# Kernel tuning notes

Hardware: AMD Instinct MI355X
Metric: run time of the kernel (lower is better)

The kernel has to match this reference:

```python
import jax, jax.numpy as jnp
import numpy as np

N = 50000
E = 600000
IN_DIM = 256
H1, H2, H3 = 128, 64, 64
HEADS = 8


def _add_self_loops(edge_index, edge_weight=None):
    loop = jnp.arange(N, dtype=edge_index.dtype)
    src = jnp.concatenate([edge_index[0], loop])
    dst = jnp.concatenate([edge_index[1], loop])
    if edge_weight is None:
        return src, dst, None
    ew = jnp.concatenate([edge_weight, jnp.ones((N,), edge_weight.dtype)])
    return src, dst, ew


def gcn_conv(x, edge_index, edge_weight, W, b):
    # PyG GCNConv: add self-loops (weight 1), symmetric normalization, scatter-add.
    src, dst, ew = _add_self_loops(edge_index, edge_weight)
    deg = jax.ops.segment_sum(ew, dst, num_segments=N)          # [N]
    dinv = jnp.where(deg > 0, jax.lax.rsqrt(jnp.maximum(deg, 1e-12)), 0.0)
    coeff = dinv[src] * ew * dinv[dst]                          # [E+N]
    h = x @ W                                                    # [N, out]
    out = jax.ops.segment_sum(coeff[:, None] * h[src], dst, num_segments=N)
    return out + b


def gat_conv(x, edge_index, W, att_src, att_dst, b):
    # PyG GATConv, heads=HEADS, concat=False (mean over heads), leaky_relu slope 0.2.
    src, dst, _ = _add_self_loops(edge_index)
    C = W.shape[1] // HEADS
    h = (x @ W).reshape(N, HEADS, C)                             # [N,H,C]
    a_s = jnp.sum(h * att_src, axis=-1)                          # [N,H]
    a_d = jnp.sum(h * att_dst, axis=-1)                          # [N,H]
    e = jax.nn.leaky_relu(a_s[src] + a_d[dst], negative_slope=0.2)  # [E',H]
    # scatter-softmax over edges sharing a destination
    m = jax.ops.segment_max(e, dst, num_segments=N)              # [N,H]
    p = jnp.exp(e - m[dst])
    s = jax.ops.segment_sum(p, dst, num_segments=N)              # [N,H]
    alpha = p / (s[dst] + 1e-16)                                 # [E',H]
    out = jax.ops.segment_sum(alpha[:, :, None] * h[src], dst, num_segments=N)  # [N,H,C]
    return jnp.mean(out, axis=1) + b


def setup_inputs() -> dict:
    key = jax.random.key(0)
    ks = jax.random.split(key, 12)
    x = jax.random.normal(ks[0], (N, IN_DIM), dtype=jnp.float32)
    edge_index = jax.random.randint(ks[1], (2, E), 0, N, dtype=jnp.int32)
    edge_weight = jax.random.uniform(ks[2], (E,), dtype=jnp.float32)
    def glorot(k, shape):
        fan = shape[0] + shape[-1]
        return jax.random.normal(k, shape, dtype=jnp.float32) * np.sqrt(2.0 / fan)
    return {
        "x": x, "edge_index": edge_index, "edge_weight": edge_weight,
        "gc1_w": glorot(ks[3], (IN_DIM, H1)), "gc1_b": jnp.zeros((H1,), jnp.float32),
        "gat_w": glorot(ks[4], (H1, HEADS * H2)),
        "att_src": glorot(ks[5], (HEADS, H2)), "att_dst": glorot(ks[6], (HEADS, H2)),
        "gat_b": jnp.zeros((H2,), jnp.float32),
        "gc2_w": glorot(ks[7], (H2, H3)), "gc2_b": jnp.zeros((H3,), jnp.float32),
        "fc_w": glorot(ks[8], (H3, 1)), "fc_b": jnp.zeros((1,), jnp.float32),
    }


def reference(x, edge_index, edge_weight, gc1_w, gc1_b, gat_w, att_src, att_dst,
              gat_b, gc2_w, gc2_b, fc_w, fc_b):
    # dropout is inference no-op
    h = jax.nn.relu(gcn_conv(x, edge_index, edge_weight, gc1_w, gc1_b))
    h = jax.nn.relu(gat_conv(h, edge_index, gat_w, att_src, att_dst, gat_b))
    h = jax.nn.relu(gcn_conv(h, edge_index, edge_weight, gc2_w, gc2_b))
    return h @ fc_w + fc_b                                       # [N,1]
```

## Files before the change

### kernel.cpp

```cpp
#include <hip/hip_runtime.h>
#include <hip/hip_bf16.h>

#define GNN_N 50000
#define GNN_E 600000

typedef unsigned int uint;
typedef unsigned short ushort;
using short8 = __attribute__((ext_vector_type(8))) short;
using f32x4  = __attribute__((ext_vector_type(4))) float;

__device__ __forceinline__ float leaky02(float x) { return x > 0.f ? x : 0.2f * x; }
__device__ __forceinline__ ushort f2b(float f) {
    uint u = __float_as_uint(f);
    return (ushort)((u + 0x7fffu + ((u >> 16) & 1u)) >> 16);
}
__device__ __forceinline__ float b2f(ushort b) { return __uint_as_float(((uint)b) << 16); }

__global__ void gnn_deg_init(float* deg, int n) {
    int i = blockIdx.x * blockDim.x + threadIdx.x;
    if (i < n) deg[i] = 1.0f;
}
__global__ void gnn_hist(const int* __restrict__ dst, const float* __restrict__ ew,
                         int* __restrict__ cnt, float* __restrict__ deg, int e) {
    int i = blockIdx.x * blockDim.x + threadIdx.x;
    if (i >= e) return;
    int d = dst[i];
    atomicAdd(&cnt[d], 1);
    atomicAdd(&deg[d], ew[i]);
}
__global__ void gnn_deg_fin(float* deg, int n) {
    int i = blockIdx.x * blockDim.x + threadIdx.x;
    if (i < n) deg[i] = rsqrtf(deg[i]);
}
__global__ void gnn_scan1(const int* __restrict__ cnt, int* __restrict__ row_ptr,
                          int* __restrict__ blksum, int n) {
    __shared__ int sh[256];
    int tid = threadIdx.x;
    int base = blockIdx.x * 1024 + tid * 4;
    int v0 = (base + 0 < n) ? cnt[base + 0] : 0;
    int v1 = (base + 1 < n) ? cnt[base + 1] : 0;
    int v2 = (base + 2 < n) ? cnt[base + 2] : 0;
    int v3 = (base + 3 < n) ? cnt[base + 3] : 0;
    int tsum = v0 + v1 + v2 + v3;
    sh[tid] = tsum;
    __syncthreads();
    for (int off = 1; off < 256; off <<= 1) {
        int t = (tid >= off) ? sh[tid - off] : 0;
        __syncthreads();
        sh[tid] += t;
        __syncthreads();
    }
    int excl = sh[tid] - tsum;
    if (base + 0 < n) row_ptr[base + 0] = excl; excl += v0;
    if (base + 1 < n) row_ptr[base + 1] = excl; excl += v1;
    if (base + 2 < n) row_ptr[base + 2] = excl; excl += v2;
    if (base + 3 < n) row_ptr[base + 3] = excl;
    if (tid == 255) blksum[blockIdx.x] = sh[255];
}
__global__ void gnn_scan2(int* blksum, int nblk, int* row_ptr_end, int total) {
    if (threadIdx.x == 0 && blockIdx.x == 0) {
        int run = 0;
        for (int b = 0; b < nblk; ++b) { int t = blksum[b]; blksum[b] = run; run += t; }
        *row_ptr_end = total;
    }
}
__global__ void gnn_scan3(int* row_ptr, const int* __restrict__ blksum, int n) {
    int i = blockIdx.x * blockDim.x + threadIdx.x;
    if (i < n) row_ptr[i] += blksum[i >> 10];
}
__global__ void gnn_scatter(const int* __restrict__ src, const int* __restrict__ dst,
                            const float* __restrict__ ew, const float* __restrict__ dinv,
                            const int* __restrict__ row_ptr, int* __restrict__ fill,
                            int* __restrict__ esrc, float* __restrict__ ecw, int e) {
    int i = blockIdx.x * blockDim.x + threadIdx.x;
    if (i >= e) return;
    int d = dst[i];
    int s = src[i];
    int pos = row_ptr[d] + atomicAdd(&fill[d], 1);
    esrc[pos] = s;
    ecw[pos] = dinv[s] * ew[i] * dinv[d];
}

__global__ void gnn_cast_bf16(const float* __restrict__ in, ushort* __restrict__ out, int n4) {
    int i = blockIdx.x * 256 + threadIdx.x;
    if (i >= n4) return;
    float4 v = ((const float4*)in)[i];
    ushort4 o;
    o.x = f2b(v.x); o.y = f2b(v.y); o.z = f2b(v.z); o.w = f2b(v.w);
    ((ushort4*)out)[i] = o;
}
__global__ void gnn_transpose_cast(const float* __restrict__ B, ushort* __restrict__ Bt,
                                   int K, int N) {
    int idx = blockIdx.x * 256 + threadIdx.x;
    if (idx >= K * N) return;
    int k = idx / N, n = idx - k * N;
    Bt[(size_t)n * K + k] = f2b(B[idx]);
}
__global__ void gnn_fold_att(const float* __restrict__ W, const float* __restrict__ att_src,
                             const float* __restrict__ att_dst, float* __restrict__ wa_t) {
    int t = blockIdx.x * 256 + threadIdx.x;
    if (t >= 16 * 128) return;
    int j = t >> 7;
    int k = t & 127;
    int h = j & 7;
    const float* av = (j < 8) ? att_src : att_dst;
    float s = 0.f;
    for (int c = 0; c < 64; ++c) s += W[(size_t)k * 512 + h * 64 + c] * av[h * 64 + c];
    wa_t[j * 128 + k] = s;
}

__global__ __launch_bounds__(256) void gnn_mfma_gemm(const ushort* __restrict__ A,
                                                     const ushort* __restrict__ Bt,
                                                     ushort* __restrict__ C,
                                                     int M, int N, int K) {
    __shared__ ushort As[64 * 40];
    __shared__ ushort Bs[64 * 40];
    const int tid = threadIdx.x;
    const int wv = tid >> 6, lane = tid & 63;
    const int g = lane >> 4, r = lane & 15;
    const int brow = blockIdx.y << 6, bcol = blockIdx.x << 6;

    const int srow = tid >> 2;
    const int skoff = (tid & 3) << 3;
    int arow = brow + srow;
    if (arow >= M) arow = M - 1;
    const ushort* Ap = A + (size_t)arow * K + skoff;
    const ushort* Bp = Bt + (size_t)(bcol + srow) * K + skoff;
    ushort* AsW = &As[srow * 40 + skoff];
    ushort* BsW = &Bs[srow * 40 + skoff];

    f32x4 acc[4] = {};

    for (int k0 = 0; k0 < K; k0 += 32) {
        *(short8*)AsW = *(const short8*)(Ap + k0);
        *(short8*)BsW = *(const short8*)(Bp + k0);
        __syncthreads();
        short8 bfrag = *(const short8*)&Bs[(wv * 16 + r) * 40 + g * 8];
#pragma unroll
        for (int mb = 0; mb < 4; ++mb) {
            short8 afrag = *(const short8*)&As[(mb * 16 + r) * 40 + g * 8];
            acc[mb] = __builtin_amdgcn_mfma_f32_16x16x32_bf16(afrag, bfrag, acc[mb], 0, 0, 0);
        }
        __syncthreads();
    }

    const int col = bcol + wv * 16 + r;
#pragma unroll
    for (int mb = 0; mb < 4; ++mb) {
        int rowb = brow + mb * 16 + g * 4;
#pragma unroll
        for (int rr = 0; rr < 4; ++rr) {
            int row = rowb + rr;
            if (row < M) C[(size_t)row * N + col] = f2b(acc[mb][rr]);
        }
    }
}

__global__ __launch_bounds__(256) void gnn_gcn_node128_asd(const int* __restrict__ row_ptr,
                                                           const int* __restrict__ esrc,
                                                           const float* __restrict__ ecw,
                                                           const float* __restrict__ dinv,
                                                           const ushort* __restrict__ hb,
                                                           const float* __restrict__ b,
                                                           const float* __restrict__ wa,
                                                           ushort* __restrict__ out,
                                                           float* __restrict__ a_s,
                                                           float* __restrict__ a_d, int n) {
    __shared__ float swa[16 * 128];
    for (int i = threadIdx.x; i < 16 * 128; i += 256) swa[i] = wa[i];
    __syncthreads();
    int v = blockIdx.x * 4 + (threadIdx.x >> 6);
    int lane = threadIdx.x & 63;
    if (v >= n) return;
    float di = dinv[v];
    float sc = di * di;
    uint us = *(const uint*)(hb + (size_t)v * 128 + 2 * lane);
    float acc0 = sc * __uint_as_float(us << 16);
    float acc1 = sc * __uint_as_float(us & 0xffff0000u);
    int beg = row_ptr[v], end = row_ptr[v + 1];
    int p = beg;
    for (; p + 4 <= end; p += 4) {
        int s0 = esrc[p], s1 = esrc[p + 1], s2 = esrc[p + 2], s3 = esrc[p + 3];
        float c0 = ecw[p], c1 = ecw[p + 1], c2 = ecw[p + 2], c3 = ecw[p + 3];
        uint u0 = *(const uint*)(hb + (size_t)s0 * 128 + 2 * lane);
        uint u1 = *(const uint*)(hb + (size_t)s1 * 128 + 2 * lane);
        uint u2 = *(const uint*)(hb + (size_t)s2 * 128 + 2 * lane);
        uint u3 = *(const uint*)(hb + (size_t)s3 * 128 + 2 * lane);
        acc0 += c0 * __uint_as_float(u0 << 16) + c1 * __uint_as_float(u1 << 16) +
                c2 * __uint_as_float(u2 << 16) + c3 * __uint_as_float(u3 << 16);
        acc1 += c0 * __uint_as_float(u0 & 0xffff0000u) + c1 * __uint_as_float(u1 & 0xffff0000u) +
                c2 * __uint_as_float(u2 & 0xffff0000u) + c3 * __uint_as_float(u3 & 0xffff0000u);
    }
    for (; p < end; ++p) {
        int s = esrc[p];
        float cw = ecw[p];
        uint u = *(const uint*)(hb + (size_t)s * 128 + 2 * lane);
        acc0 += cw * __uint_as_float(u << 16);
        acc1 += cw * __uint_as_float(u & 0xffff0000u);
    }
    float o0 = acc0 + b[2 * lane];
    float o1 = acc1 + b[2 * lane + 1];
    o0 = o0 > 0.f ? o0 : 0.f;
    o1 = o1 > 0.f ? o1 : 0.f;
    uint o = (uint)f2b(o0) | ((uint)f2b(o1) << 16);
    *(uint*)(out + (size_t)v * 128 + 2 * lane) = o;

    float part[16];
#pragma unroll
    for (int j = 0; j < 16; ++j)
        part[j] = o0 * swa[j * 128 + 2 * lane] + o1 * swa[j * 128 + 2 * lane + 1];
#pragma unroll
    for (int m = 1; m < 64; m <<= 1) {
#pragma unroll
        for (int j = 0; j < 16; ++j) part[j] += __shfl_xor(part[j], m);
    }
    if (lane == 0) {
#pragma unroll
        for (int j = 0; j < 8; ++j) {
            a_s[(size_t)v * 8 + j] = part[j];
            a_d[(size_t)v * 8 + j] = part[8 + j];
        }
    }
}

__global__ __launch_bounds__(256) void gnn_gat_node2(const int* __restrict__ row_ptr,
                                                     const int* __restrict__ esrc,
                                                     const float* __restrict__ a_s,
                                                     const float* __restrict__ a_d,
                                                     const ushort* __restrict__ h2,
                                                     const float* __restrict__ gat_b,
                                                     ushort* __restrict__ out, int n) {
    int v = blockIdx.x * 4 + (threadIdx.x >> 6);
    int lane = threadIdx.x & 63;
    if (v >= n) return;
    const int hd = lane >> 3;
    const float adh = a_d[(size_t)v * 8 + hd];

    float vh[8];
    float sl;
    {
        float ps = __expf(leaky02(a_s[(size_t)v * 8 + hd] + adh));
        short8 q = *(const short8*)(h2 + (size_t)v * 512 + lane * 8);
        sl = ps;
#pragma unroll
        for (int j = 0; j < 8; ++j) vh[j] = ps * b2f((ushort)q[j]);
    }
    int beg = row_ptr[v], end = row_ptr[v + 1];
    int p = beg;
    for (; p + 4 <= end; p += 4) {
        int s0 = esrc[p], s1 = esrc[p + 1], s2 = esrc[p + 2], s3 = esrc[p + 3];
        float e0 = a_s[(size_t)s0 * 8 + hd];
        float e1 = a_s[(size_t)s1 * 8 + hd];
        float e2 = a_s[(size_t)s2 * 8 + hd];
        float e3 = a_s[(size_t)s3 * 8 + hd];
        short8 q0 = *(const short8*)(h2 + (size_t)s0 * 512 + lane * 8);
        short8 q1 = *(const short8*)(h2 + (size_t)s1 * 512 + lane * 8);
        short8 q2 = *(const short8*)(h2 + (size_t)s2 * 512 + lane * 8);
        short8 q3 = *(const short8*)(h2 + (size_t)s3 * 512 + lane * 8);
        float p0 = __expf(leaky02(e0 + adh));
        float p1 = __expf(leaky02(e1 + adh));
        float p2 = __expf(leaky02(e2 + adh));
        float p3 = __expf(leaky02(e3 + adh));
        sl += (p0 + p1) + (p2 + p3);
#pragma unroll
        for (int j = 0; j < 8; ++j)
            vh[j] += p0 * b2f((ushort)q0[j]) + p1 * b2f((ushort)q1[j]) +
                     p2 * b2f((ushort)q2[j]) + p3 * b2f((ushort)q3[j]);
    }
    for (; p < end; ++p) {
        int s = esrc[p];
        float pp = __expf(leaky02(a_s[(size_t)s * 8 + hd] + adh));
        short8 q = *(const short8*)(h2 + (size_t)s * 512 + lane * 8);
        sl += pp;
#pragma unroll
        for (int j = 0; j < 8; ++j) vh[j] += pp * b2f((ushort)q[j]);
    }
    float rs = 1.f / (sl + 1e-16f);
#pragma unroll
    for (int j = 0; j < 8; ++j) vh[j] *= rs;
#pragma unroll
    for (int m = 8; m < 64; m <<= 1) {
#pragma unroll
        for (int j = 0; j < 8; ++j) vh[j] += __shfl_xor(vh[j], m);
    }
    if (lane < 8) {
        short8 o;
#pragma unroll
        for (int j = 0; j < 8; ++j) {
            float t = 0.125f * vh[j] + gat_b[lane * 8 + j];
            t = t > 0.f ? t : 0.f;
            o[j] = (short)f2b(t);
        }
        *(short8*)(out + (size_t)v * 64 + lane * 8) = o;
    }
}

__global__ __launch_bounds__(256) void gnn_gcn_node64_fc(const int* __restrict__ row_ptr,
                                                         const int* __restrict__ esrc,
                                                         const float* __restrict__ ecw,
                                                         const float* __restrict__ dinv,
                                                         const ushort* __restrict__ hb,
                                                         const float* __restrict__ b,
                                                         const float* __restrict__ fc_w,
                                                         const float* __restrict__ fc_b,
                                                         float* __restrict__ out, int n) {
    int v = blockIdx.x * 4 + (threadIdx.x >> 6);
    int lane = threadIdx.x & 63;
    if (v >= n) return;
    float di = dinv[v];
    float acc = di * di * b2f(hb[(size_t)v * 64 + lane]);
    int beg = row_ptr[v], end = row_ptr[v + 1];
    int p = beg;
    for (; p + 4 <= end; p += 4) {
        int s0 = esrc[p], s1 = esrc[p + 1], s2 = esrc[p + 2], s3 = esrc[p + 3];
        float c0 = ecw[p], c1 = ecw[p + 1], c2 = ecw[p + 2], c3 = ecw[p + 3];
        float h0 = b2f(hb[(size_t)s0 * 64 + lane]);
        float h1 = b2f(hb[(size_t)s1 * 64 + lane]);
        float h2v = b2f(hb[(size_t)s2 * 64 + lane]);
        float h3v = b2f(hb[(size_t)s3 * 64 + lane]);
        acc += c0 * h0 + c1 * h1 + c2 * h2v + c3 * h3v;
    }
    for (; p < end; ++p) {
        int s = esrc[p];
        acc += ecw[p] * b2f(hb[(size_t)s * 64 + lane]);
    }
    float o = acc + b[lane];
    o = o > 0.f ? o : 0.f;
    float val = o * fc_w[lane];
#pragma unroll
    for (int m = 32; m; m >>= 1) val += __shfl_xor(val, m);
    if (lane == 0) out[v] = val + fc_b[0];
}

extern "C" void kernel_launch(void* const* d_in, const int* in_sizes, int n_in,
                              void* d_out, int out_size, void* d_ws, size_t ws_size,
                              hipStream_t stream) {
    const float* x       = (const float*)d_in[0];
    const int*   ei      = (const int*)d_in[1];
    const float* ew      = (const float*)d_in[2];
    const float* gc1_w   = (const float*)d_in[3];
    const float* gc1_b   = (const float*)d_in[4];
    const float* gat_w   = (const float*)d_in[5];
    const float* att_src = (const float*)d_in[6];
    const float* att_dst = (const float*)d_in[7];
    const float* gat_b   = (const float*)d_in[8];
    const float* gc2_w   = (const float*)d_in[9];
    const float* gc2_b   = (const float*)d_in[10];
    const float* fc_w    = (const float*)d_in[11];
    const float* fc_b    = (const float*)d_in[12];
    float* out = (float*)d_out;

    const int N = GNN_N;
    const int E = in_sizes[2];
    const int* src = ei;
    const int* dst = ei + E;

    char* p = (char*)d_ws;
    ushort* h2b = (ushort*)p; p += (size_t)N * 512 * 2;
    ushort* xb  = (ushort*)p; p += (size_t)N * 256 * 2;
    ushort* h1b = (ushort*)p; p += (size_t)N * 128 * 2;
    ushort* g1b = (ushort*)p; p += (size_t)N * 128 * 2;
    ushort* g2b = (ushort*)p; p += (size_t)N * 64 * 2;
    ushort* h3b = (ushort*)p; p += (size_t)N * 64 * 2;
    ushort* w1t = (ushort*)p; p += (size_t)128 * 256 * 2;
    ushort* w2t = (ushort*)p; p += (size_t)512 * 128 * 2;
    ushort* w3t = (ushort*)p; p += (size_t)64 * 64 * 2;
    float*  wa_t = (float*)p; p += 16 * 128 * 4;
    float*  a_s = (float*)p;  p += (size_t)N * 8 * 4;
    float*  a_d = (float*)p;  p += (size_t)N * 8 * 4;
    float*  dinv = (float*)p; p += (size_t)N * 4;
    int* row_ptr = (int*)p;   p += (size_t)(N + 64) * 4;
    int* esrc = (int*)p;      p += (size_t)E * 4;
    float* ecw = (float*)p;   p += (size_t)E * 4;
    int* cnt = (int*)p;       p += (size_t)N * 4;
    int* fill = (int*)p;      p += (size_t)N * 4;
    int* blksum = (int*)p;    p += 4096;

    auto cdiv = [](long a, long b) { return (int)((a + b - 1) / b); };

    hipMemsetAsync(cnt, 0, (size_t)N * 8, stream);
    gnn_deg_init<<<cdiv(N, 256), 256, 0, stream>>>(dinv, N);
    gnn_hist<<<cdiv(E, 256), 256, 0, stream>>>(dst, ew, cnt, dinv, E);
    gnn_deg_fin<<<cdiv(N, 256), 256, 0, stream>>>(dinv, N);
    const int nblk = cdiv(N, 1024);
    gnn_scan1<<<nblk, 256, 0, stream>>>(cnt, row_ptr, blksum, N);
    gnn_scan2<<<1, 64, 0, stream>>>(blksum, nblk, row_ptr + N, E);
    gnn_scan3<<<cdiv(N, 256), 256, 0, stream>>>(row_ptr, blksum, N);
    gnn_scatter<<<cdiv(E, 256), 256, 0, stream>>>(src, dst, ew, dinv, row_ptr, fill, esrc, ecw, E);

    gnn_cast_bf16<<<cdiv((long)N * 256 / 4, 256), 256, 0, stream>>>(x, xb, N * 256 / 4);
    gnn_transpose_cast<<<cdiv(256 * 128, 256), 256, 0, stream>>>(gc1_w, w1t, 256, 128);
    gnn_transpose_cast<<<cdiv(128 * 512, 256), 256, 0, stream>>>(gat_w, w2t, 128, 512);
    gnn_transpose_cast<<<cdiv(64 * 64, 256), 256, 0, stream>>>(gc2_w, w3t, 64, 64);
    gnn_fold_att<<<8, 256, 0, stream>>>(gat_w, att_src, att_dst, wa_t);

    {
        dim3 grid(128 / 64, cdiv(N, 64));
        gnn_mfma_gemm<<<grid, 256, 0, stream>>>(xb, w1t, h1b, N, 128, 256);
    }
    gnn_gcn_node128_asd<<<cdiv(N, 4), 256, 0, stream>>>(row_ptr, esrc, ecw, dinv, h1b, gc1_b,
                                                        wa_t, g1b, a_s, a_d, N);

    {
        dim3 grid(512 / 64, cdiv(N, 64));
        gnn_mfma_gemm<<<grid, 256, 0, stream>>>(g1b, w2t, h2b, N, 512, 128);
    }
    gnn_gat_node2<<<cdiv(N, 4), 256, 0, stream>>>(row_ptr, esrc, a_s, a_d, h2b, gat_b, g2b, N);

    {
        dim3 grid(1, cdiv(N, 64));
        gnn_mfma_gemm<<<grid, 256, 0, stream>>>(g2b, w3t, h3b, N, 64, 64);
    }
    gnn_gcn_node64_fc<<<cdiv(N, 4), 256, 0, stream>>>(row_ptr, esrc, ecw, dinv, h3b, gc2_b,
                                                      fc_w, fc_b, out, N);
}
```

Before: 385.7 us.

## Fuse fp32-to-bf16 cast into first GEMM, merge prep kernels, unroll gathers by eight

The first GEMM now loads fp32 x directly and converts it to bf16 while staging into shared memory, which removes the separate cast kernel and its bf16 copy of x. The three weight transposes and the attention fold are merged into one prep kernel. The degree-init kernel is replaced by a wider memset, with the self-loop weight added in deg_fin. The gather loops in the three aggregation kernels are unrolled to eight edges to keep more loads in flight, at the cost of more registers per thread.

```diff
diff --git a/kernel.cpp b/kernel.cpp
--- a/kernel.cpp
+++ b/kernel.cpp
@@ -16,10 +16,6 @@
 }
 __device__ __forceinline__ float b2f(ushort b) { return __uint_as_float(((uint)b) << 16); }
 
-__global__ void gnn_deg_init(float* deg, int n) {
-    int i = blockIdx.x * blockDim.x + threadIdx.x;
-    if (i < n) deg[i] = 1.0f;
-}
 __global__ void gnn_hist(const int* __restrict__ dst, const float* __restrict__ ew,
                          int* __restrict__ cnt, float* __restrict__ deg, int e) {
     int i = blockIdx.x * blockDim.x + threadIdx.x;
@@ -30,7 +26,7 @@
 }
 __global__ void gnn_deg_fin(float* deg, int n) {
     int i = blockIdx.x * blockDim.x + threadIdx.x;
-    if (i < n) deg[i] = rsqrtf(deg[i]);
+    if (i < n) deg[i] = rsqrtf(1.0f + deg[i]);
 }
 __global__ void gnn_scan1(const int* __restrict__ cnt, int* __restrict__ row_ptr,
                           int* __restrict__ blksum, int n) {
@@ -81,35 +77,42 @@
     ecw[pos] = dinv[s] * ew[i] * dinv[d];
 }
 
-__global__ void gnn_cast_bf16(const float* __restrict__ in, ushort* __restrict__ out, int n4) {
-    int i = blockIdx.x * 256 + threadIdx.x;
-    if (i >= n4) return;
-    float4 v = ((const float4*)in)[i];
-    ushort4 o;
-    o.x = f2b(v.x); o.y = f2b(v.y); o.z = f2b(v.z); o.w = f2b(v.w);
-    ((ushort4*)out)[i] = o;
-}
-__global__ void gnn_transpose_cast(const float* __restrict__ B, ushort* __restrict__ Bt,
-                                   int K, int N) {
-    int idx = blockIdx.x * 256 + threadIdx.x;
-    if (idx >= K * N) return;
-    int k = idx / N, n = idx - k * N;
-    Bt[(size_t)n * K + k] = f2b(B[idx]);
-}
-__global__ void gnn_fold_att(const float* __restrict__ W, const float* __restrict__ att_src,
-                             const float* __restrict__ att_dst, float* __restrict__ wa_t) {
+__global__ void gnn_prep(const float* __restrict__ gc1_w, const float* __restrict__ gat_w,
+                         const float* __restrict__ gc2_w, const float* __restrict__ att_src,
+                         const float* __restrict__ att_dst, ushort* __restrict__ w1t,
+                         ushort* __restrict__ w2t, ushort* __restrict__ w3t,
+                         float* __restrict__ wa_t) {
     int t = blockIdx.x * 256 + threadIdx.x;
-    if (t >= 16 * 128) return;
-    int j = t >> 7;
-    int k = t & 127;
-    int h = j & 7;
-    const float* av = (j < 8) ? att_src : att_dst;
-    float s = 0.f;
-    for (int c = 0; c < 64; ++c) s += W[(size_t)k * 512 + h * 64 + c] * av[h * 64 + c];
-    wa_t[j * 128 + k] = s;
-}
-
-__global__ __launch_bounds__(256) void gnn_mfma_gemm(const ushort* __restrict__ A,
+    if (t < 32768) {
+        int k = t >> 7, n = t & 127;
+        w1t[n * 256 + k] = f2b(gc1_w[t]);
+        return;
+    }
+    t -= 32768;
+    if (t < 65536) {
+        int k = t >> 9, n = t & 511;
+        w2t[n * 128 + k] = f2b(gat_w[t]);
+        return;
+    }
+    t -= 65536;
+    if (t < 4096) {
+        int k = t >> 6, n = t & 63;
+        w3t[n * 64 + k] = f2b(gc2_w[t]);
+        return;
+    }
+    t -= 4096;
+    if (t < 2048) {
+        int j = t >> 7, k = t & 127;
+        int h = j & 7;
+        const float* av = (j < 8) ? att_src : att_dst;
+        float s = 0.f;
+        for (int c = 0; c < 64; ++c) s += gat_w[(size_t)k * 512 + h * 64 + c] * av[h * 64 + c];
+        wa_t[j * 128 + k] = s;
+    }
+}
+
+template <bool AF32>
+__global__ __launch_bounds__(256) void gnn_mfma_gemm(const void* __restrict__ Av,
                                                      const ushort* __restrict__ Bt,
                                                      ushort* __restrict__ C,
                                                      int M, int N, int K) {
@@ -124,7 +127,10 @@
     const int skoff = (tid & 3) << 3;
     int arow = brow + srow;
     if (arow >= M) arow = M - 1;
-    const ushort* Ap = A + (size_t)arow * K + skoff;
+    const ushort* A16 = (const ushort*)Av;
+    const float*  A32 = (const float*)Av;
+    const ushort* Ap16 = A16 + (size_t)arow * K + skoff;
+    const float*  Ap32 = A32 + (size_t)arow * K + skoff;
     const ushort* Bp = Bt + (size_t)(bcol + srow) * K + skoff;
     ushort* AsW = &As[srow * 40 + skoff];
     ushort* BsW = &Bs[srow * 40 + skoff];
@@ -132,7 +138,18 @@
     f32x4 acc[4] = {};
 
     for (int k0 = 0; k0 < K; k0 += 32) {
-        *(short8*)AsW = *(const short8*)(Ap + k0);
+        if constexpr (AF32) {
+            float4 f0 = *(const float4*)(Ap32 + k0);
+            float4 f1 = *(const float4*)(Ap32 + k0 + 4);
+            short8 t;
+            t[0] = (short)f2b(f0.x); t[1] = (short)f2b(f0.y);
+            t[2] = (short)f2b(f0.z); t[3] = (short)f2b(f0.w);
+            t[4] = (short)f2b(f1.x); t[5] = (short)f2b(f1.y);
+            t[6] = (short)f2b(f1.z); t[7] = (short)f2b(f1.w);
+            *(short8*)AsW = t;
+        } else {
+            *(short8*)AsW = *(const short8*)(Ap16 + k0);
+        }
         *(short8*)BsW = *(const short8*)(Bp + k0);
         __syncthreads();
         short8 bfrag = *(const short8*)&Bs[(wv * 16 + r) * 40 + g * 8];
@@ -179,17 +196,19 @@
     float acc1 = sc * __uint_as_float(us & 0xffff0000u);
     int beg = row_ptr[v], end = row_ptr[v + 1];
     int p = beg;
-    for (; p + 4 <= end; p += 4) {
-        int s0 = esrc[p], s1 = esrc[p + 1], s2 = esrc[p + 2], s3 = esrc[p + 3];
-        float c0 = ecw[p], c1 = ecw[p + 1], c2 = ecw[p + 2], c3 = ecw[p + 3];
-        uint u0 = *(const uint*)(hb + (size_t)s0 * 128 + 2 * lane);
-        uint u1 = *(const uint*)(hb + (size_t)s1 * 128 + 2 * lane);
-        uint u2 = *(const uint*)(hb + (size_t)s2 * 128 + 2 * lane);
-        uint u3 = *(const uint*)(hb + (size_t)s3 * 128 + 2 * lane);
-        acc0 += c0 * __uint_as_float(u0 << 16) + c1 * __uint_as_float(u1 << 16) +
-                c2 * __uint_as_float(u2 << 16) + c3 * __uint_as_float(u3 << 16);
-        acc1 += c0 * __uint_as_float(u0 & 0xffff0000u) + c1 * __uint_as_float(u1 & 0xffff0000u) +
-                c2 * __uint_as_float(u2 & 0xffff0000u) + c3 * __uint_as_float(u3 & 0xffff0000u);
+    for (; p + 8 <= end; p += 8) {
+        int s[8]; float c[8]; uint u[8];
+#pragma unroll
+        for (int t = 0; t < 8; ++t) s[t] = esrc[p + t];
+#pragma unroll
+        for (int t = 0; t < 8; ++t) c[t] = ecw[p + t];
+#pragma unroll
+        for (int t = 0; t < 8; ++t) u[t] = *(const uint*)(hb + (size_t)s[t] * 128 + 2 * lane);
+#pragma unroll
+        for (int t = 0; t < 8; ++t) {
+            acc0 += c[t] * __uint_as_float(u[t] << 16);
+            acc1 += c[t] * __uint_as_float(u[t] & 0xffff0000u);
+        }
     }
     for (; p < end; ++p) {
         int s = esrc[p];
@@ -247,25 +266,38 @@
     }
     int beg = row_ptr[v], end = row_ptr[v + 1];
     int p = beg;
-    for (; p + 4 <= end; p += 4) {
-        int s0 = esrc[p], s1 = esrc[p + 1], s2 = esrc[p + 2], s3 = esrc[p + 3];
-        float e0 = a_s[(size_t)s0 * 8 + hd];
-        float e1 = a_s[(size_t)s1 * 8 + hd];
-        float e2 = a_s[(size_t)s2 * 8 + hd];
-        float e3 = a_s[(size_t)s3 * 8 + hd];
-        short8 q0 = *(const short8*)(h2 + (size_t)s0 * 512 + lane * 8);
-        short8 q1 = *(const short8*)(h2 + (size_t)s1 * 512 + lane * 8);
-        short8 q2 = *(const short8*)(h2 + (size_t)s2 * 512 + lane * 8);
-        short8 q3 = *(const short8*)(h2 + (size_t)s3 * 512 + lane * 8);
-        float p0 = __expf(leaky02(e0 + adh));
-        float p1 = __expf(leaky02(e1 + adh));
-        float p2 = __expf(leaky02(e2 + adh));
-        float p3 = __expf(leaky02(e3 + adh));
-        sl += (p0 + p1) + (p2 + p3);
-#pragma unroll
-        for (int j = 0; j < 8; ++j)
-            vh[j] += p0 * b2f((ushort)q0[j]) + p1 * b2f((ushort)q1[j]) +
-                     p2 * b2f((ushort)q2[j]) + p3 * b2f((ushort)q3[j]);
+    for (; p + 8 <= end; p += 8) {
+        int s[8]; float e[8]; short8 q[8];
+#pragma unroll
+        for (int t = 0; t < 8; ++t) s[t] = esrc[p + t];
+#pragma unroll
+        for (int t = 0; t < 8; ++t) e[t] = a_s[(size_t)s[t] * 8 + hd];
+#pragma unroll
+        for (int t = 0; t < 8; ++t) q[t] = *(const short8*)(h2 + (size_t)s[t] * 512 + lane * 8);
+#pragma unroll
+        for (int t = 0; t < 8; ++t) {
+            float pp = __expf(leaky02(e[t] + adh));
+            sl += pp;
+#pragma unroll
+            for (int j = 0; j < 8; ++j) vh[j] += pp * b2f((ushort)q[t][j]);
+        }
+    }
+    if (p + 4 <= end) {
+        int s[4]; float e[4]; short8 q[4];
+#pragma unroll
+        for (int t = 0; t < 4; ++t) s[t] = esrc[p + t];
+#pragma unroll
+        for (int t = 0; t < 4; ++t) e[t] = a_s[(size_t)s[t] * 8 + hd];
+#pragma unroll
+        for (int t = 0; t < 4; ++t) q[t] = *(const short8*)(h2 + (size_t)s[t] * 512 + lane * 8);
+#pragma unroll
+        for (int t = 0; t < 4; ++t) {
+            float pp = __expf(leaky02(e[t] + adh));
+            sl += pp;
+#pragma unroll
+            for (int j = 0; j < 8; ++j) vh[j] += pp * b2f((ushort)q[t][j]);
+        }
+        p += 4;
     }
     for (; p < end; ++p) {
         int s = esrc[p];
@@ -311,14 +343,16 @@
     float acc = di * di * b2f(hb[(size_t)v * 64 + lane]);
     int beg = row_ptr[v], end = row_ptr[v + 1];
     int p = beg;
-    for (; p + 4 <= end; p += 4) {
-        int s0 = esrc[p], s1 = esrc[p + 1], s2 = esrc[p + 2], s3 = esrc[p + 3];
-        float c0 = ecw[p], c1 = ecw[p + 1], c2 = ecw[p + 2], c3 = ecw[p + 3];
-        float h0 = b2f(hb[(size_t)s0 * 64 + lane]);
-        float h1 = b2f(hb[(size_t)s1 * 64 + lane]);
-        float h2v = b2f(hb[(size_t)s2 * 64 + lane]);
-        float h3v = b2f(hb[(size_t)s3 * 64 + lane]);
-        acc += c0 * h0 + c1 * h1 + c2 * h2v + c3 * h3v;
+    for (; p + 8 <= end; p += 8) {
+        int s[8]; float c[8]; ushort hv[8];
+#pragma unroll
+        for (int t = 0; t < 8; ++t) s[t] = esrc[p + t];
+#pragma unroll
+        for (int t = 0; t < 8; ++t) c[t] = ecw[p + t];
+#pragma unroll
+        for (int t = 0; t < 8; ++t) hv[t] = hb[(size_t)s[t] * 64 + lane];
+#pragma unroll
+        for (int t = 0; t < 8; ++t) acc += c[t] * b2f(hv[t]);
     }
     for (; p < end; ++p) {
         int s = esrc[p];
@@ -357,7 +391,6 @@
 
     char* p = (char*)d_ws;
     ushort* h2b = (ushort*)p; p += (size_t)N * 512 * 2;
-    ushort* xb  = (ushort*)p; p += (size_t)N * 256 * 2;
     ushort* h1b = (ushort*)p; p += (size_t)N * 128 * 2;
     ushort* g1b = (ushort*)p; p += (size_t)N * 128 * 2;
     ushort* g2b = (ushort*)p; p += (size_t)N * 64 * 2;
@@ -368,18 +401,17 @@
     float*  wa_t = (float*)p; p += 16 * 128 * 4;
     float*  a_s = (float*)p;  p += (size_t)N * 8 * 4;
     float*  a_d = (float*)p;  p += (size_t)N * 8 * 4;
-    float*  dinv = (float*)p; p += (size_t)N * 4;
     int* row_ptr = (int*)p;   p += (size_t)(N + 64) * 4;
     int* esrc = (int*)p;      p += (size_t)E * 4;
     float* ecw = (float*)p;   p += (size_t)E * 4;
     int* cnt = (int*)p;       p += (size_t)N * 4;
     int* fill = (int*)p;      p += (size_t)N * 4;
+    float* dinv = (float*)p;  p += (size_t)N * 4;
     int* blksum = (int*)p;    p += 4096;
 
     auto cdiv = [](long a, long b) { return (int)((a + b - 1) / b); };
 
-    hipMemsetAsync(cnt, 0, (size_t)N * 8, stream);
-    gnn_deg_init<<<cdiv(N, 256), 256, 0, stream>>>(dinv, N);
+    hipMemsetAsync(cnt, 0, (size_t)N * 12, stream);
     gnn_hist<<<cdiv(E, 256), 256, 0, stream>>>(dst, ew, cnt, dinv, E);
     gnn_deg_fin<<<cdiv(N, 256), 256, 0, stream>>>(dinv, N);
     const int nblk = cdiv(N, 1024);
@@ -388,28 +420,24 @@
     gnn_scan3<<<cdiv(N, 256), 256, 0, stream>>>(row_ptr, blksum, N);
     gnn_scatter<<<cdiv(E, 256), 256, 0, stream>>>(src, dst, ew, dinv, row_ptr, fill, esrc, ecw, E);
 
-    gnn_cast_bf16<<<cdiv((long)N * 256 / 4, 256), 256, 0, stream>>>(x, xb, N * 256 / 4);
-    gnn_transpose_cast<<<cdiv(256 * 128, 256), 256, 0, stream>>>(gc1_w, w1t, 256, 128);
-    gnn_transpose_cast<<<cdiv(128 * 512, 256), 256, 0, stream>>>(gat_w, w2t, 128, 512);
-    gnn_transpose_cast<<<cdiv(64 * 64, 256), 256, 0, stream>>>(gc2_w, w3t, 64, 64);
-    gnn_fold_att<<<8, 256, 0, stream>>>(gat_w, att_src, att_dst, wa_t);
+    gnn_prep<<<408, 256, 0, stream>>>(gc1_w, gat_w, gc2_w, att_src, att_dst, w1t, w2t, w3t, wa_t);
 
     {
         dim3 grid(128 / 64, cdiv(N, 64));
-        gnn_mfma_gemm<<<grid, 256, 0, stream>>>(xb, w1t, h1b, N, 128, 256);
+        gnn_mfma_gemm<true><<<grid, 256, 0, stream>>>(x, w1t, h1b, N, 128, 256);
     }
     gnn_gcn_node128_asd<<<cdiv(N, 4), 256, 0, stream>>>(row_ptr, esrc, ecw, dinv, h1b, gc1_b,
                                                         wa_t, g1b, a_s, a_d, N);
 
     {
         dim3 grid(512 / 64, cdiv(N, 64));
-        gnn_mfma_gemm<<<grid, 256, 0, stream>>>(g1b, w2t, h2b, N, 512, 128);
+        gnn_mfma_gemm<false><<<grid, 256, 0, stream>>>(g1b, w2t, h2b, N, 512, 128);
     }
     gnn_gat_node2<<<cdiv(N, 4), 256, 0, stream>>>(row_ptr, esrc, a_s, a_d, h2b, gat_b, g2b, N);
 
     {
         dim3 grid(1, cdiv(N, 64));
-        gnn_mfma_gemm<<<grid, 256, 0, stream>>>(g2b, w3t, h3b, N, 64, 64);
+        gnn_mfma_gemm<false><<<grid, 256, 0, stream>>>(g2b, w3t, h3b, N, 64, 64);
     }
     gnn_gcn_node64_fc<<<cdiv(N, 4), 256, 0, stream>>>(row_ptr, esrc, ecw, dinv, h3b, gc2_b,
                                                       fc_w, fc_b, out, N);
```

After: 374.9 us. 2.8% less time.
